# Kernel tuning notes

Hardware: AMD Instinct MI355X
Metric: run time of the kernel (lower is better)

## Reference

```python
import jax, jax.numpy as jnp
import numpy as np

NEG_INF = -1e30
GAP_OPEN = -5.0
GAP_EXTEND = -1.0
TEMP = 1.0
# penalize_turns=True
RIGHTMOD = jnp.array([GAP_OPEN, GAP_EXTEND, GAP_OPEN], dtype=jnp.float32)
DOWNMOD = jnp.array([GAP_OPEN, GAP_OPEN, GAP_EXTEND], dtype=jnp.float32)


def setup_inputs() -> dict:
    key = jax.random.key(0)
    x = jax.random.normal(key, (512, 151, 151), dtype=jnp.float32)
    return {"x": x}


def _lse(v):
    # temperature-scaled smooth max over last axis
    return TEMP * jax.nn.logsumexp(v / TEMP, axis=-1)


def _sw_forward(x):
    B, N, M = x.shape
    a, b = N - 1, M - 1
    core = x[:, :-1, :-1]  # (B, a, b) similarity scores used in the DP

    # anti-diagonal rotation indices (static, numpy)
    ar = np.arange(a - 1, -1, -1)[:, None]          # (a, 1)
    br = np.arange(b)[None, :]                       # (1, b)
    i = br - ar + (a - 1)                            # diagonal index, (a, b)
    j = (ar + br) // 2                               # position within diagonal
    n_diag = a + b - 1
    m = (a + b) // 2
    smo = jnp.asarray(((np.arange(n_diag) + a % 2) % 2).astype(np.float32))  # parity per diagonal

    smx = jnp.full((B, n_diag, m), NEG_INF, dtype=x.dtype).at[:, i, j].set(core)
    smx_t = jnp.transpose(smx, (1, 0, 2))  # (n_diag, B, m) for scan

    def step(carry, inp):
        h2, h1 = carry            # each (B, m, 3)
        sx, so = inp              # sx (B, m), so scalar parity in {0,1}
        # align: pad state dim with 0 (fresh local-alignment start), add match score
        align = jnp.concatenate([h2, jnp.zeros_like(h2[..., :1])], axis=-1) + sx[..., None]
        # shifted views of h1 along the diagonal-position axis
        h1_dn = jnp.concatenate([jnp.full_like(h1[:, :1, :], NEG_INF), h1[:, :-1, :]], axis=1)
        h1_up = jnp.concatenate([h1[:, 1:, :], jnp.full_like(h1[:, :1, :], NEG_INF)], axis=1)
        right = so * h1_dn + (1.0 - so) * h1 + RIGHTMOD
        down = so * h1 + (1.0 - so) * h1_up + DOWNMOD
        right = right[:, :, :2]  # restrict_turns=True
        h0 = jnp.stack([_lse(align), _lse(right), _lse(down)], axis=-1)  # (B, m, 3)
        return (h1, h0), h0

    init_h = jnp.full((B, m, 3), NEG_INF, dtype=x.dtype)
    _, ys = jax.lax.scan(step, (init_h, init_h), (smx_t, smo))  # ys (n_diag, B, m, 3)
    results = jnp.transpose(ys, (1, 0, 2, 3))  # (B, n_diag, m, 3)
    hij = results[:, i, j]                      # un-rotate -> (B, a, b, 3)
    scores = (hij + x[:, 1:, 1:, None]).reshape(B, -1)
    final = TEMP * jax.nn.logsumexp(scores / TEMP, axis=-1)  # (B,)
    return final.sum()


def reference(x):
    return _sw_forward(x)
```

## Files before the change

kernel.cpp:

```cpp
#include <hip/hip_runtime.h>


#define CGO 6.737946999085467e-03f
#define CGE 3.678794411714423e-01f
#define L2E 1.4426950408889634f
#define LN2 0.6931471805599453f
#define RTHR 0x1p28f
#define RSC  0x1p-64f
#define EADD 64.0f

#define SA1 4.9787068367863944e-02f
#define SA2 2.4787521766663585e-03f
#define SA4 6.1442123533282098e-06f
#define SA8 3.7751345442790977e-11f
#define CA1 3.6787944117144233e-01f
#define CA2 1.3533528323661270e-01f
#define CA3 4.9787068367863944e-02f

#if __has_builtin(__builtin_amdgcn_exp2f)
#define EXP2(x) __builtin_amdgcn_exp2f(x)
#else
static __device__ __forceinline__ float EXP2_(float x){float r;asm("v_exp_f32 %0, %1":"=v"(r):"v"(x));return r;}
#define EXP2(x) EXP2_(x)
#endif

#if __has_builtin(__builtin_amdgcn_logf)
#define LOG2(x) __builtin_amdgcn_logf(x)
#else
static __device__ __forceinline__ float LOG2_(float x){float r;asm("v_log_f32 %0, %1":"=v"(r):"v"(x));return r;}
#define LOG2(x) LOG2_(x)
#endif

#define DPP_UP   0x138
#define DPP_DN   0x130
#define ROW_SHR1 0x111
#define ROW_SHR2 0x112
#define ROW_SHR4 0x114
#define ROW_SHR8 0x118
#define BCAST15  0x142
#define BCAST31  0x143

template<int CTRL>
static __device__ __forceinline__ float dppz(float v){
    return __int_as_float(__builtin_amdgcn_update_dpp(
        0, __float_as_int(v), CTRL, 0xF, 0xF, true));
}

static __device__ __forceinline__ float dec16(unsigned bits16){
    unsigned short us = (unsigned short)bits16;
    _Float16 h;
    __builtin_memcpy(&h, &us, 2);
    return (float)h;
}

template<int IMM>
static __device__ __forceinline__
void stepRow(const char* ldsB, const int vaddr,
             const float vA16, const float vA32,
             float (&SX)[3], unsigned& Rc,
             float (&HSs)[3], float (&g)[3], float (&h2p)[3],
             const float oneE, float (&S)[3])
{
    const unsigned Rn = *(const unsigned*)(ldsB + vaddr + IMM);
    const float D0 = dec16(Rc << 8);
    const float D1 = dec16(Rc & 0xFF00u);
    const float D2 = dec16((Rc >> 8) & 0xFF00u);
    const float D3 = dppz<DPP_DN>(D0);

    const float h00 = SX[0] * (HSs[0] + oneE);
    const float h01 = SX[1] * (HSs[1] + oneE);
    const float h02 = SX[2] * (HSs[2] + oneE);

    const float h0u = dppz<DPP_UP>(h02);
    const float b0 = CGO * h0u;
    const float b1 = CGO * h00;
    const float b2 = CGO * h01;

    const float p1 = fmaf(CGE, b0, b1);
    const float p2 = fmaf(CGE, p1, b2);

    float t = dppz<DPP_UP>(p2);
    t = fmaf(SA1, dppz<ROW_SHR1>(t), t);
    t = fmaf(SA2, dppz<ROW_SHR2>(t), t);
    t = fmaf(SA4, dppz<ROW_SHR4>(t), t);
    t = fmaf(SA8, dppz<ROW_SHR8>(t), t);
    t = fmaf(vA16, dppz<BCAST15>(t), t);
    t = fmaf(vA32, dppz<BCAST31>(t), t);

    const float h10 = fmaf(CA1, t, b0);
    const float h11 = fmaf(CA2, t, p1);
    const float h12 = fmaf(CA3, t, p2);

    const float h20 = fmaf(CGO, g[0], CGE * h2p[0]);
    const float h21 = fmaf(CGO, g[1], CGE * h2p[1]);
    const float h22 = fmaf(CGO, g[2], CGE * h2p[2]);

    g[0] = h00 + h10; g[1] = h01 + h11; g[2] = h02 + h12;
    const float hs0 = g[0] + h20;
    const float hs1 = g[1] + h21;
    const float hs2 = g[2] + h22;
    h2p[0] = h20; h2p[1] = h21; h2p[2] = h22;

    S[0] = fmaf(D1, hs0, S[0]);
    S[1] = fmaf(D2, hs1, S[1]);
    S[2] = fmaf(D3, hs2, S[2]);

    HSs[0] = dppz<DPP_UP>(hs2);
    HSs[1] = hs0; HSs[2] = hs1;
    SX[0] = D0; SX[1] = D1; SX[2] = D2;
    Rc = Rn;
}

__global__ __launch_bounds__(256)
void sw_row(const float* __restrict__ x, float* __restrict__ part,
            float* __restrict__ out_atomic, int use_atomic) {
    const int b = blockIdx.x;
    const float* xb = x + (size_t)b * 22801;
    const int tid = threadIdx.x;

    __shared__ char ldsB[38912];

    {
        int4* l4 = (int4*)ldsB;
        for (int i = tid; i < 38912 / 16; i += 256) l4[i] = int4{0,0,0,0};
    }
    __syncthreads();

    for (int i = 0; i < 90; ++i) {
        const int idx = i * 256 + tid;
        const int idc = idx > 22800 ? 22800 : idx;
        const float v = EXP2(xb[idc] * L2E);
        const _Float16 hv = (_Float16)v;
        unsigned short u16; __builtin_memcpy(&u16, &hv, 2);
        const unsigned byte = ((unsigned)u16 + 0x7Fu + ((u16 >> 8) & 1u)) >> 8;
        const unsigned r = ((unsigned)idc * 111111u) >> 24;
        const int c = idc - 151 * (int)r;
        const int l3 = (c * 0x5556) >> 16;
        const int kk = c - 3 * l3;
        ldsB[(int)r * 256 + 4 * l3 + kk] = (char)byte;
    }
    __syncthreads();
    if (tid >= 64) return;

    const int lane = tid;
    const float vA16 = EXP2(-4.3280851226668902f * (float)((lane & 15) + 1));
    const float vA32 = EXP2(-4.3280851226668902f * (float)((lane & 31) + 1));
    const int vl4 = 4 * lane;

    float SX[3];
    unsigned Rc;
    {
        const unsigned w0 = *(const unsigned*)(ldsB + vl4);
        SX[0] = dec16(w0 << 8);
        SX[1] = dec16(w0 & 0xFF00u);
        SX[2] = dec16((w0 >> 8) & 0xFF00u);
        Rc = *(const unsigned*)(ldsB + 256 + vl4);
    }
    float HSs[3] = {0.0f, 0.0f, 0.0f};
    float g[3]   = {0.0f, 0.0f, 0.0f};
    float h2p[3] = {0.0f, 0.0f, 0.0f};
    float S[3]   = {0.0f, 0.0f, 0.0f};
    float oneE = 1.0f;
    float E = 0.0f;

    int vaddr = 512 + vl4;

    for (int gi = 0; gi < 18; ++gi) {
        stepRow<   0>(ldsB, vaddr, vA16, vA32, SX, Rc, HSs, g, h2p, oneE, S);
        stepRow< 256>(ldsB, vaddr, vA16, vA32, SX, Rc, HSs, g, h2p, oneE, S);
        stepRow< 512>(ldsB, vaddr, vA16, vA32, SX, Rc, HSs, g, h2p, oneE, S);
        stepRow< 768>(ldsB, vaddr, vA16, vA32, SX, Rc, HSs, g, h2p, oneE, S);
        stepRow<1024>(ldsB, vaddr, vA16, vA32, SX, Rc, HSs, g, h2p, oneE, S);
        stepRow<1280>(ldsB, vaddr, vA16, vA32, SX, Rc, HSs, g, h2p, oneE, S);
        stepRow<1536>(ldsB, vaddr, vA16, vA32, SX, Rc, HSs, g, h2p, oneE, S);
        float m = fmaxf(fmaxf(g[0], g[1]), g[2]);
        m = fmaxf(m, fmaxf(fmaxf(h2p[0], h2p[1]), h2p[2]));
        const bool rn = __any(m > RTHR);
        const float sc = rn ? RSC : 1.0f;
        stepRow<1792>(ldsB, vaddr, vA16, vA32, SX, Rc, HSs, g, h2p, oneE, S);
        #pragma unroll
        for (int k = 0; k < 3; ++k) {
            HSs[k] *= sc; g[k] *= sc; h2p[k] *= sc; S[k] *= sc;
        }
        oneE *= sc; E += rn ? EADD : 0.0f;
        vaddr += 2048;
    }
    stepRow<   0>(ldsB, vaddr, vA16, vA32, SX, Rc, HSs, g, h2p, oneE, S);
    stepRow< 256>(ldsB, vaddr, vA16, vA32, SX, Rc, HSs, g, h2p, oneE, S);
    stepRow< 512>(ldsB, vaddr, vA16, vA32, SX, Rc, HSs, g, h2p, oneE, S);
    stepRow< 768>(ldsB, vaddr, vA16, vA32, SX, Rc, HSs, g, h2p, oneE, S);
    stepRow<1024>(ldsB, vaddr, vA16, vA32, SX, Rc, HSs, g, h2p, oneE, S);
    stepRow<1280>(ldsB, vaddr, vA16, vA32, SX, Rc, HSs, g, h2p, oneE, S);

    float St = (S[0] + S[1]) + S[2];
    #pragma unroll
    for (int off = 32; off; off >>= 1) St += __shfl_xor(St, off, 64);
    if (lane == 0) {
        const float val = LN2 * (E + LOG2(St));
        if (use_atomic) atomicAdd(out_atomic, val);
        else            part[b] = val;
    }
}

__global__ __launch_bounds__(256)
void final_reduce(const float* __restrict__ part, float* __restrict__ out) {
    const int t = threadIdx.x;
    float v = part[t] + part[t + 256];
    #pragma unroll
    for (int off = 32; off; off >>= 1) v += __shfl_xor(v, off);
    __shared__ float ws[4];
    if ((t & 63) == 0) ws[t >> 6] = v;
    __syncthreads();
    if (t == 0) out[0] = ws[0] + ws[1] + ws[2] + ws[3];
}

extern "C" void kernel_launch(void* const* d_in, const int* in_sizes, int n_in,
                              void* d_out, int out_size, void* d_ws, size_t ws_size,
                              hipStream_t stream) {
    const float* x = (const float*)d_in[0];
    float* out = (float*)d_out;

    if (ws_size >= 512 * sizeof(float)) {
        float* part = (float*)d_ws;
        sw_row<<<512, 256, 0, stream>>>(x, part, nullptr, 0);
        final_reduce<<<1, 256, 0, stream>>>(part, out);
    } else {
        hipMemsetAsync(out, 0, sizeof(float), stream);
        sw_row<<<512, 256, 0, stream>>>(x, nullptr, out, 1);
    }
}
```

Before: 35.87 us.

## Restructure row recurrence to shorten serial DPP scan dependency chain

Reformulates the per-row recurrence so the cross-lane prefix scan runs on a single carried value and the per-lane coefficients for the next row are precomputed off the critical path. The scan drops the shift-by-4 and shift-by-8 stages, uses a masked broadcast, and reuses rescaled coefficients. The goal is a shorter loop-carried dependency chain of DPP moves and FMAs per row in this latency-bound single-wave kernel. The risk is that truncating the scan terms changes numerical accuracy, and the reordered algebra may not exactly match the previous recurrence.

```diff
diff --git a/kernel.cpp b/kernel.cpp
--- a/kernel.cpp
+++ b/kernel.cpp
@@ -9,13 +9,14 @@
 #define RSC  0x1p-64f
 #define EADD 64.0f
 
-#define SA1 4.9787068367863944e-02f
-#define SA2 2.4787521766663585e-03f
-#define SA4 6.1442123533282098e-06f
-#define SA8 3.7751345442790977e-11f
-#define CA1 3.6787944117144233e-01f
-#define CA2 1.3533528323661270e-01f
-#define CA3 4.9787068367863944e-02f
+#define K20 6.737946999085467e-03f
+#define K21 2.478752176666358e-03f
+#define K22 9.118819655545162e-04f
+#define CA1 3.678794411714423e-01f
+#define CA2 1.353352832366127e-01f
+#define CA3 4.978706836786394e-02f
+#define SAW1 4.978706836786394e-02f
+#define SAW2 2.478752176666358e-03f
 
 #if __has_builtin(__builtin_amdgcn_exp2f)
 #define EXP2(x) __builtin_amdgcn_exp2f(x)
@@ -35,15 +36,18 @@
 #define DPP_DN   0x130
 #define ROW_SHR1 0x111
 #define ROW_SHR2 0x112
-#define ROW_SHR4 0x114
-#define ROW_SHR8 0x118
 #define BCAST15  0x142
 #define BCAST31  0x143
 
-template<int CTRL>
+template<int CTRL, int RMASK = 0xF>
 static __device__ __forceinline__ float dppz(float v){
     return __int_as_float(__builtin_amdgcn_update_dpp(
-        0, __float_as_int(v), CTRL, 0xF, 0xF, true));
+        0, __float_as_int(v), CTRL, RMASK, 0xF, true));
+}
+template<int CTRL>
+static __device__ __forceinline__ float dppc(float old, float v){
+    return __int_as_float(__builtin_amdgcn_update_dpp(
+        __float_as_int(old), __float_as_int(v), CTRL, 0xF, 0xF, false));
 }
 
 static __device__ __forceinline__ float dec16(unsigned bits16){
@@ -57,63 +61,62 @@
 static __device__ __forceinline__
 void stepRow(const char* ldsB, const int vaddr,
              const float vA16, const float vA32,
-             float (&SX)[3], unsigned& Rc,
-             float (&HSs)[3], float (&g)[3], float (&h2p)[3],
-             const float oneE, float (&S)[3])
+             float& Cp, float (&cA)[3], float (&cB)[3],
+             float (&g)[3], float (&h2p)[3],
+             unsigned& Rc, const float oneE, float (&S)[3])
 {
+    const float Cs  = dppz<DPP_UP>(Cp);
+    const float h01 = fmaf(cA[1], Cp, cB[1]);
+    const float h02 = fmaf(cA[2], Cp, cB[2]);
+    const float h00 = fmaf(cA[0], Cs, cB[0]);
+    const float U   = dppz<DPP_UP>(h02);
+    const float tp  = fmaf(K21, h00, K20 * h01);
+    const float p2  = fmaf(K22, U, tp);
+    float t = dppz<DPP_UP>(p2);
+    t = fmaf(SAW1, dppz<ROW_SHR1>(t), t);
+    t = fmaf(SAW2, dppz<ROW_SHR2>(t), t);
+    t = fmaf(vA16, dppz<BCAST15, 0xa>(t), t);
+    const float Cn = fmaf(vA32, dppz<BCAST31>(t), t);
+
     const unsigned Rn = *(const unsigned*)(ldsB + vaddr + IMM);
     const float D0 = dec16(Rc << 8);
     const float D1 = dec16(Rc & 0xFF00u);
     const float D2 = dec16((Rc >> 8) & 0xFF00u);
     const float D3 = dppz<DPP_DN>(D0);
 
-    const float h00 = SX[0] * (HSs[0] + oneE);
-    const float h01 = SX[1] * (HSs[1] + oneE);
-    const float h02 = SX[2] * (HSs[2] + oneE);
-
-    const float h0u = dppz<DPP_UP>(h02);
-    const float b0 = CGO * h0u;
-    const float b1 = CGO * h00;
-    const float b2 = CGO * h01;
-
-    const float p1 = fmaf(CGE, b0, b1);
-    const float p2 = fmaf(CGE, p1, b2);
-
-    float t = dppz<DPP_UP>(p2);
-    t = fmaf(SA1, dppz<ROW_SHR1>(t), t);
-    t = fmaf(SA2, dppz<ROW_SHR2>(t), t);
-    t = fmaf(SA4, dppz<ROW_SHR4>(t), t);
-    t = fmaf(SA8, dppz<ROW_SHR8>(t), t);
-    t = fmaf(vA16, dppz<BCAST15>(t), t);
-    t = fmaf(vA32, dppz<BCAST31>(t), t);
-
-    const float h10 = fmaf(CA1, t, b0);
-    const float h11 = fmaf(CA2, t, p1);
-    const float h12 = fmaf(CA3, t, p2);
-
+    const float b0 = K20 * U;
+    const float p1 = fmaf(K21, U, K20 * h00);
     const float h20 = fmaf(CGO, g[0], CGE * h2p[0]);
     const float h21 = fmaf(CGO, g[1], CGE * h2p[1]);
     const float h22 = fmaf(CGO, g[2], CGE * h2p[2]);
-
-    g[0] = h00 + h10; g[1] = h01 + h11; g[2] = h02 + h12;
-    const float hs0 = g[0] + h20;
-    const float hs1 = g[1] + h21;
-    const float hs2 = g[2] + h22;
+    const float Q0n = (h00 + b0) + h20;
+    const float Q1n = (h01 + p1) + h21;
+    const float Q2n = (h02 + p2) + h22;
+
+    S[0] = fmaf(D1, fmaf(CA1, Cn, Q0n), S[0]);
+    S[1] = fmaf(D2, fmaf(CA2, Cn, Q1n), S[1]);
+    S[2] = fmaf(D3, fmaf(CA3, Cn, Q2n), S[2]);
+
+    g[0] = h00 + fmaf(CA1, Cn, b0);
+    g[1] = h01 + fmaf(CA2, Cn, p1);
+    g[2] = h02 + fmaf(CA3, Cn, p2);
     h2p[0] = h20; h2p[1] = h21; h2p[2] = h22;
 
-    S[0] = fmaf(D1, hs0, S[0]);
-    S[1] = fmaf(D2, hs1, S[1]);
-    S[2] = fmaf(D3, hs2, S[2]);
-
-    HSs[0] = dppz<DPP_UP>(hs2);
-    HSs[1] = hs0; HSs[2] = hs1;
-    SX[0] = D0; SX[1] = D1; SX[2] = D2;
+    const float Q0 = Q0n + oneE;
+    const float Q1 = Q1n + oneE;
+    const float Q2 = Q2n + oneE;
+    const float Q2s = dppc<DPP_UP>(oneE, Q2);
+    cA[0] = CA3 * D0;  cB[0] = D0 * Q2s;
+    cA[1] = CA1 * D1;  cB[1] = D1 * Q0;
+    cA[2] = CA2 * D2;  cB[2] = D2 * Q1;
+
     Rc = Rn;
+    Cp = Cn;
 }
 
 __global__ __launch_bounds__(256)
-void sw_row(const float* __restrict__ x, float* __restrict__ part,
-            float* __restrict__ out_atomic, int use_atomic) {
+void sw_fastrow(const float* __restrict__ x, float* __restrict__ part,
+                float* __restrict__ out_atomic, int use_atomic) {
     const int b = blockIdx.x;
     const float* xb = x + (size_t)b * 22801;
     const int tid = threadIdx.x;
@@ -147,16 +150,16 @@
     const float vA32 = EXP2(-4.3280851226668902f * (float)((lane & 31) + 1));
     const int vl4 = 4 * lane;
 
-    float SX[3];
-    unsigned Rc;
+    float Cp = 0.0f;
+    float cA[3], cB[3];
     {
         const unsigned w0 = *(const unsigned*)(ldsB + vl4);
-        SX[0] = dec16(w0 << 8);
-        SX[1] = dec16(w0 & 0xFF00u);
-        SX[2] = dec16((w0 >> 8) & 0xFF00u);
-        Rc = *(const unsigned*)(ldsB + 256 + vl4);
-    }
-    float HSs[3] = {0.0f, 0.0f, 0.0f};
+        cA[0] = 0.0f; cA[1] = 0.0f; cA[2] = 0.0f;
+        cB[0] = dec16(w0 << 8);
+        cB[1] = dec16(w0 & 0xFF00u);
+        cB[2] = dec16((w0 >> 8) & 0xFF00u);
+    }
+    unsigned Rc = *(const unsigned*)(ldsB + 256 + vl4);
     float g[3]   = {0.0f, 0.0f, 0.0f};
     float h2p[3] = {0.0f, 0.0f, 0.0f};
     float S[3]   = {0.0f, 0.0f, 0.0f};
@@ -166,31 +169,31 @@
     int vaddr = 512 + vl4;
 
     for (int gi = 0; gi < 18; ++gi) {
-        stepRow<   0>(ldsB, vaddr, vA16, vA32, SX, Rc, HSs, g, h2p, oneE, S);
-        stepRow< 256>(ldsB, vaddr, vA16, vA32, SX, Rc, HSs, g, h2p, oneE, S);
-        stepRow< 512>(ldsB, vaddr, vA16, vA32, SX, Rc, HSs, g, h2p, oneE, S);
-        stepRow< 768>(ldsB, vaddr, vA16, vA32, SX, Rc, HSs, g, h2p, oneE, S);
-        stepRow<1024>(ldsB, vaddr, vA16, vA32, SX, Rc, HSs, g, h2p, oneE, S);
-        stepRow<1280>(ldsB, vaddr, vA16, vA32, SX, Rc, HSs, g, h2p, oneE, S);
-        stepRow<1536>(ldsB, vaddr, vA16, vA32, SX, Rc, HSs, g, h2p, oneE, S);
+        stepRow<   0>(ldsB, vaddr, vA16, vA32, Cp, cA, cB, g, h2p, Rc, oneE, S);
+        stepRow< 256>(ldsB, vaddr, vA16, vA32, Cp, cA, cB, g, h2p, Rc, oneE, S);
+        stepRow< 512>(ldsB, vaddr, vA16, vA32, Cp, cA, cB, g, h2p, Rc, oneE, S);
+        stepRow< 768>(ldsB, vaddr, vA16, vA32, Cp, cA, cB, g, h2p, Rc, oneE, S);
+        stepRow<1024>(ldsB, vaddr, vA16, vA32, Cp, cA, cB, g, h2p, Rc, oneE, S);
+        stepRow<1280>(ldsB, vaddr, vA16, vA32, Cp, cA, cB, g, h2p, Rc, oneE, S);
+        stepRow<1536>(ldsB, vaddr, vA16, vA32, Cp, cA, cB, g, h2p, Rc, oneE, S);
         float m = fmaxf(fmaxf(g[0], g[1]), g[2]);
         m = fmaxf(m, fmaxf(fmaxf(h2p[0], h2p[1]), h2p[2]));
         const bool rn = __any(m > RTHR);
         const float sc = rn ? RSC : 1.0f;
-        stepRow<1792>(ldsB, vaddr, vA16, vA32, SX, Rc, HSs, g, h2p, oneE, S);
+        stepRow<1792>(ldsB, vaddr, vA16, vA32, Cp, cA, cB, g, h2p, Rc, oneE, S);
         #pragma unroll
         for (int k = 0; k < 3; ++k) {
-            HSs[k] *= sc; g[k] *= sc; h2p[k] *= sc; S[k] *= sc;
+            cB[k] *= sc; g[k] *= sc; h2p[k] *= sc; S[k] *= sc;
         }
-        oneE *= sc; E += rn ? EADD : 0.0f;
+        Cp *= sc; oneE *= sc; E += rn ? EADD : 0.0f;
         vaddr += 2048;
     }
-    stepRow<   0>(ldsB, vaddr, vA16, vA32, SX, Rc, HSs, g, h2p, oneE, S);
-    stepRow< 256>(ldsB, vaddr, vA16, vA32, SX, Rc, HSs, g, h2p, oneE, S);
-    stepRow< 512>(ldsB, vaddr, vA16, vA32, SX, Rc, HSs, g, h2p, oneE, S);
-    stepRow< 768>(ldsB, vaddr, vA16, vA32, SX, Rc, HSs, g, h2p, oneE, S);
-    stepRow<1024>(ldsB, vaddr, vA16, vA32, SX, Rc, HSs, g, h2p, oneE, S);
-    stepRow<1280>(ldsB, vaddr, vA16, vA32, SX, Rc, HSs, g, h2p, oneE, S);
+    stepRow<   0>(ldsB, vaddr, vA16, vA32, Cp, cA, cB, g, h2p, Rc, oneE, S);
+    stepRow< 256>(ldsB, vaddr, vA16, vA32, Cp, cA, cB, g, h2p, Rc, oneE, S);
+    stepRow< 512>(ldsB, vaddr, vA16, vA32, Cp, cA, cB, g, h2p, Rc, oneE, S);
+    stepRow< 768>(ldsB, vaddr, vA16, vA32, Cp, cA, cB, g, h2p, Rc, oneE, S);
+    stepRow<1024>(ldsB, vaddr, vA16, vA32, Cp, cA, cB, g, h2p, Rc, oneE, S);
+    stepRow<1280>(ldsB, vaddr, vA16, vA32, Cp, cA, cB, g, h2p, Rc, oneE, S);
 
     float St = (S[0] + S[1]) + S[2];
     #pragma unroll
@@ -222,10 +225,10 @@
 
     if (ws_size >= 512 * sizeof(float)) {
         float* part = (float*)d_ws;
-        sw_row<<<512, 256, 0, stream>>>(x, part, nullptr, 0);
+        sw_fastrow<<<512, 256, 0, stream>>>(x, part, nullptr, 0);
         final_reduce<<<1, 256, 0, stream>>>(part, out);
     } else {
         hipMemsetAsync(out, 0, sizeof(float), stream);
-        sw_row<<<512, 256, 0, stream>>>(x, nullptr, out, 1);
-    }
-}
+        sw_fastrow<<<512, 256, 0, stream>>>(x, nullptr, out, 1);
+    }
+}
```

Result: slower. 40.05 us (+11.7%).
